# Optimization experiments

Measured on AMD Instinct MI355X. Metric: run time of the kernel, lower is better.

Reference implementation:

```python
import jax, jax.numpy as jnp
import numpy as np

D = 256; H = 8; L = 4; K = 4; AS = 2; HD = D // H
KK = K * K
LEVEL_SHAPES = [(128, 128), (64, 64), (32, 32), (16, 16)]


def _kernel_indices():
    # kernel_size=4 (even): linspace(-1.5, 1.5, 4); stack [j, i] then / K
    idx = jnp.linspace(-1.5, 1.5, K)
    ii, jj = jnp.meshgrid(idx, idx, indexing='ij')
    return jnp.stack([jj, ii], axis=-1).reshape(-1, 2) / K  # (KK, 2)


def _bilinear(vf, g, Hl, Wl):
    # vf: (b, H, Hl*Wl, HD) per-level value; g: (b, l1, H, KK, 2) in [0,1]
    # grid_sample semantics, align_corners=False, zero padding
    b, l1, h, kk, _ = g.shape
    x = g[..., 0] * Wl - 0.5
    y = g[..., 1] * Hl - 0.5
    x0 = jnp.floor(x)
    y0 = jnp.floor(y)
    acc = None
    for dx, dy in ((0, 0), (1, 0), (0, 1), (1, 1)):
        xi = x0 + dx
        yi = y0 + dy
        w = (1.0 - jnp.abs(x - xi)) * (1.0 - jnp.abs(y - yi))
        valid = (xi >= 0) & (xi < Wl) & (yi >= 0) & (yi < Hl)
        idx = (jnp.clip(yi, 0, Hl - 1) * Wl + jnp.clip(xi, 0, Wl - 1)).astype(jnp.int32)
        idx = idx.transpose(0, 2, 1, 3).reshape(b, h, l1 * kk)
        gth = jnp.take_along_axis(vf, idx[..., None], axis=2)  # (b,H,l1*kk,HD)
        ww = (w * valid).transpose(0, 2, 1, 3).reshape(b, h, l1 * kk)
        c = gth * ww[..., None]
        acc = c if acc is None else acc + c
    return acc.reshape(b, h, l1, kk, HD).transpose(0, 2, 1, 3, 4)  # (b,l1,H,kk,HD)


def setup_inputs() -> dict:
    key = jax.random.key(0)
    ks = jax.random.split(key, 9)
    b, l1 = 4, 1024
    l2 = sum(h * w for h, w in LEVEL_SHAPES)  # 21760
    query = jax.random.normal(ks[0], (b, l1, D), jnp.float32)
    value = jax.random.normal(ks[1], (b, l2, D), jnp.float32)
    centers = jax.random.uniform(ks[2], (b, l1, 2), jnp.float32)
    sizes = jax.random.uniform(ks[3], (b, l1, 2), jnp.float32) * 0.2 + 0.05
    ref_windows = jnp.concatenate([centers, sizes], axis=-1)  # (b,l1,4) cx,cy,w,h
    s = 1.0 / np.sqrt(D)
    Wv = jax.random.normal(ks[4], (D, D), jnp.float32) * s
    bv = jnp.zeros((D,), jnp.float32)
    Wo = jax.random.normal(ks[5], (D, D), jnp.float32) * s
    bo = jnp.zeros((D,), jnp.float32)
    Wbox = jax.random.normal(ks[6], (L * H * 4, D), jnp.float32) * 0.01
    bbox = jax.random.uniform(ks[7], (H * L * 4,), jnp.float32)
    Wattn = jax.random.normal(ks[8], (H * L * AS * AS, D), jnp.float32) * s
    battn = jnp.zeros((H * L * AS * AS,), jnp.float32)
    v_shape = np.array(LEVEL_SHAPES, np.int64)
    starts = np.cumsum([0] + [h * w for h, w in LEVEL_SHAPES[:-1]])
    v_start_index = np.array(starts, np.int64)
    v_mask = jnp.zeros((b, l2), bool)
    return dict(query=query, value=value, ref_windows=ref_windows, Wv=Wv, bv=bv,
                Wo=Wo, bo=bo, Wbox=Wbox, bbox=bbox, Wattn=Wattn, battn=battn,
                v_shape=v_shape, v_start_index=v_start_index, v_mask=v_mask)


def reference(query, value, ref_windows, Wv, bv, Wo, bo, Wbox, bbox, Wattn, battn,
              v_shape, v_start_index, v_mask):
    b, l1, _ = query.shape
    l2 = value.shape[1]
    # value projection + padding mask
    v = value @ Wv.T + bv
    v = jnp.where(v_mask[..., None], 0.0, v).reshape(b, l2, H, HD)
    # where to attend: offset boxes -> sampling grid (normalizer=None branch)
    off = (query @ Wbox.T + bbox).reshape(b, l1, H, L, 4)
    refw = ref_windows[:, :, None, None, :]            # (b,l1,1,1,4)
    refsz = jnp.concatenate([refw[..., 2:4], refw[..., 2:4]], axis=-1)
    boxes = refw + off / 8.0 * refsz                   # (b,l1,H,L,4)
    center = boxes[..., None, :2]
    size = boxes[..., None, 2:]
    grid = center + _kernel_indices() * jax.nn.relu(size)  # (b,l1,H,L,KK,2)
    # attention weights (attn_size grid upsampled to kernel_size by repeat_interleave)
    aw = (query @ Wattn.T + battn).reshape(b, l1, H, L, AS, AS)
    nr = K // AS
    aw = jnp.repeat(jnp.repeat(aw, nr, axis=-1), nr, axis=-2)  # (b,l1,H,L,K,K)
    sw = jax.nn.softmax(aw.reshape(b, l1, H, -1), axis=-1).reshape(b, l1, H, L, KK)
    lw = jax.nn.softmax(aw, axis=3).reshape(b, l1, H, L, KK)
    out = jnp.zeros((b, l1, H, HD), query.dtype)
    mout = jnp.zeros((b, l1, H, HD), query.dtype)
    for li in range(L):
        Hl, Wl = int(v_shape[li, 0]), int(v_shape[li, 1])
        st = int(v_start_index[li])
        vf = v[:, st:st + Hl * Wl].transpose(0, 2, 1, 3)  # (b,H,Hl*Wl,HD)
        samp = _bilinear(vf, grid[:, :, :, li], Hl, Wl)   # (b,l1,H,KK,HD)
        out = out + jnp.einsum('bqhkd,bqhk->bqhd', samp, sw[:, :, :, li])
        mout = mout + jnp.einsum('bqhkd,bqhk->bqhd', samp, lw[:, :, :, li])
    out = out.reshape(b, l1, D) @ Wo.T + bo
    mout = mout.reshape(b, l1, D) @ Wo.T + bo
    return out, mout, aw
```

## Files before the change

kernel.cpp:

```cpp
#include <hip/hip_runtime.h>
#include <hip/hip_bf16.h>


typedef __attribute__((ext_vector_type(8))) short short8;
typedef __attribute__((ext_vector_type(4))) float f32x4;
typedef __attribute__((ext_vector_type(4))) unsigned int uint4v;

__device__ __forceinline__ unsigned short f2bf(float f) {
    unsigned int u = __float_as_uint(f);
    unsigned int r = u + 0x7FFFu + ((u >> 16) & 1u);
    return (unsigned short)(r >> 16);
}
__device__ __forceinline__ unsigned int pkbf(float a, float b) {
    __hip_bfloat162 h = __float22bfloat162_rn(float2{a, b});
    return *reinterpret_cast<unsigned int*>(&h);
}
__device__ __forceinline__ short8 pack2(float4 x, float4 y) {
    uint4v u;
    u[0] = pkbf(x.x, x.y); u[1] = pkbf(x.z, x.w);
    u[2] = pkbf(y.x, y.y); u[3] = pkbf(y.z, y.w);
    return __builtin_bit_cast(short8, u);
}
__device__ __forceinline__ void gld_lds16(const float* g, float* l) {
    __builtin_amdgcn_global_load_lds(
        (const __attribute__((address_space(1))) unsigned int*)g,
        (__attribute__((address_space(3))) unsigned int*)l, 16, 0, 0);
}

__device__ __forceinline__ void storeC(float* C, size_t i, float v) { C[i] = v; }
__device__ __forceinline__ void storeC(unsigned short* C, size_t i, float v) { C[i] = f2bf(v); }

#define TILE_F 4096

template <typename OutT>
__device__ __forceinline__ void gemm_body2(
    const float* __restrict__ A, const float* __restrict__ W,
    const float* __restrict__ bias, OutT* __restrict__ C,
    int N, int bm, int bn, float* AsF, float* WsF)
{
    const int tid  = threadIdx.x;
    const int lane = tid & 63;
    const int wave = tid >> 6;
    const int wm = (wave & 1) * 64;
    const int wn = (wave >> 1) * 64;
    const int kg = lane >> 4;
    const int lm = lane & 15;

    f32x4 acc[4][4];
#pragma unroll
    for (int i = 0; i < 4; ++i)
#pragma unroll
        for (int j = 0; j < 4; ++j) {
            acc[i][j][0] = 0.f; acc[i][j][1] = 0.f;
            acc[i][j][2] = 0.f; acc[i][j][3] = 0.f;
        }

    const int g = (lane & 7) ^ (lane >> 3);
    const float* Ag = A + (size_t)(bm + 32 * wave + (lane >> 3)) * 256 + 4 * g;
    const float* Wg = W + (size_t)(bn + 32 * wave + (lane >> 3)) * 256 + 4 * g;
    const int ldsw = (32 * wave) * 32;

    const int p0 = (2 * kg) ^ (lm & 7);
    const int p1 = p0 ^ 1;
    const int abase = (wm + lm) * 8;
    const int bbase = (wn + lm) * 8;

#define STAGE_VQ(BUF, K0)                                                     \
    {                                                                         \
        _Pragma("unroll")                                                     \
        for (int j = 0; j < 4; ++j) {                                         \
            gld_lds16(Ag + (size_t)j * 8 * 256 + (K0),                        \
                      AsF + (BUF) * TILE_F + ldsw + j * 8 * 32);              \
            gld_lds16(Wg + (size_t)j * 8 * 256 + (K0),                        \
                      WsF + (BUF) * TILE_F + ldsw + j * 8 * 32);              \
        }                                                                     \
    }

#define COMPUTE_VQ(BUF)                                                       \
    {                                                                         \
        const float4* Af4 = (const float4*)(AsF + (BUF) * TILE_F);            \
        const float4* Wf4 = (const float4*)(WsF + (BUF) * TILE_F);            \
        short8 af[4], bfr[4];                                                 \
        _Pragma("unroll")                                                     \
        for (int i = 0; i < 4; ++i) {                                         \
            float4 c0 = Af4[abase + i * 128 + p0];                            \
            float4 c1 = Af4[abase + i * 128 + p1];                            \
            af[i] = pack2(c0, c1);                                            \
        }                                                                     \
        _Pragma("unroll")                                                     \
        for (int j = 0; j < 4; ++j) {                                         \
            float4 c0 = Wf4[bbase + j * 128 + p0];                            \
            float4 c1 = Wf4[bbase + j * 128 + p1];                            \
            bfr[j] = pack2(c0, c1);                                           \
        }                                                                     \
        _Pragma("unroll")                                                     \
        for (int i = 0; i < 4; ++i)                                           \
            _Pragma("unroll")                                                 \
            for (int j = 0; j < 4; ++j)                                       \
                acc[i][j] = __builtin_amdgcn_mfma_f32_16x16x32_bf16(          \
                    af[i], bfr[j], acc[i][j], 0, 0, 0);                       \
    }

    STAGE_VQ(0, 0)

    for (int it = 0; it < 7; ++it) {
        const int cur = it & 1;
        const int nxt = cur ^ 1;
        STAGE_VQ(nxt, 32 * (it + 1))
        asm volatile("s_waitcnt vmcnt(8)" ::: "memory");
        __builtin_amdgcn_s_barrier();
        COMPUTE_VQ(cur)
        asm volatile("s_waitcnt lgkmcnt(0)" ::: "memory");
        __builtin_amdgcn_s_barrier();
    }
    asm volatile("s_waitcnt vmcnt(0)" ::: "memory");
    __builtin_amdgcn_s_barrier();
    COMPUTE_VQ(1)

#undef STAGE_VQ
#undef COMPUTE_VQ

#pragma unroll
    for (int j = 0; j < 4; ++j) {
        int col = bn + wn + j * 16 + lm;
        float bcol = bias[col];
#pragma unroll
        for (int i = 0; i < 4; ++i) {
#pragma unroll
            for (int r = 0; r < 4; ++r) {
                int row = bm + wm + i * 16 + kg * 4 + r;
                storeC(C, (size_t)row * N + col, acc[i][j][r] + bcol);
            }
        }
    }
}

#define LDA 56

__device__ __forceinline__ void gemm_body_f32(
    const float* __restrict__ A, const float* __restrict__ W,
    const float* __restrict__ bias, float* __restrict__ C,
    int N, int bm, int bn, unsigned short* As, unsigned short* Ws)
{
    const int tid  = threadIdx.x;
    const int lane = tid & 63;
    const int wave = tid >> 6;
    const int wm = (wave & 1) * 64;
    const int wn = (wave >> 1) * 64;
    const int lr = tid >> 1;
    const int lh = (tid & 1) * 16;
    const int kg = lane >> 4;
    const int lm = lane & 15;

    f32x4 acc[4][4];
#pragma unroll
    for (int i = 0; i < 4; ++i)
#pragma unroll
        for (int j = 0; j < 4; ++j) {
            acc[i][j][0] = 0.f; acc[i][j][1] = 0.f;
            acc[i][j][2] = 0.f; acc[i][j][3] = 0.f;
        }

    const float* Ap = A + (size_t)(bm + lr) * 256 + lh;
    const float* Wp = W + (size_t)(bn + lr) * 256 + lh;
    unsigned short* Asp = &As[lr * LDA + lh];
    unsigned short* Wsp = &Ws[lr * LDA + lh];

    for (int k0 = 0; k0 < 256; k0 += 32) {
        float4 a0 = *(const float4*)(Ap + k0);
        float4 a1 = *(const float4*)(Ap + k0 + 4);
        float4 a2 = *(const float4*)(Ap + k0 + 8);
        float4 a3 = *(const float4*)(Ap + k0 + 12);
        float4 w0 = *(const float4*)(Wp + k0);
        float4 w1 = *(const float4*)(Wp + k0 + 4);
        float4 w2 = *(const float4*)(Wp + k0 + 8);
        float4 w3 = *(const float4*)(Wp + k0 + 12);
        __syncthreads();
        *(short8*)(Asp)     = pack2(a0, a1);
        *(short8*)(Asp + 8) = pack2(a2, a3);
        *(short8*)(Wsp)     = pack2(w0, w1);
        *(short8*)(Wsp + 8) = pack2(w2, w3);
        __syncthreads();
        short8 af[4], bfr[4];
#pragma unroll
        for (int i = 0; i < 4; ++i)
            af[i] = *(const short8*)&As[(wm + i * 16 + lm) * LDA + kg * 8];
#pragma unroll
        for (int j = 0; j < 4; ++j)
            bfr[j] = *(const short8*)&Ws[(wn + j * 16 + lm) * LDA + kg * 8];
#pragma unroll
        for (int i = 0; i < 4; ++i)
#pragma unroll
            for (int j = 0; j < 4; ++j)
                acc[i][j] = __builtin_amdgcn_mfma_f32_16x16x32_bf16(
                    af[i], bfr[j], acc[i][j], 0, 0, 0);
    }

#pragma unroll
    for (int j = 0; j < 4; ++j) {
        int col = bn + wn + j * 16 + lm;
        float bcol = bias[col];
#pragma unroll
        for (int i = 0; i < 4; ++i)
#pragma unroll
            for (int r = 0; r < 4; ++r) {
                int row = bm + wm + i * 16 + kg * 4 + r;
                C[(size_t)row * N + col] = acc[i][j][r] + bcol;
            }
    }
}

__device__ __forceinline__ void gemm_body_bf16A(
    const unsigned short* __restrict__ A, const float* __restrict__ W,
    const float* __restrict__ bias, float* __restrict__ C,
    int N, int bm, int bn, unsigned short* As, unsigned short* Ws)
{
    const int tid  = threadIdx.x;
    const int lane = tid & 63;
    const int wave = tid >> 6;
    const int wm = (wave & 1) * 64;
    const int wn = (wave >> 1) * 64;
    const int lr = tid >> 1;
    const int lh = (tid & 1) * 16;
    const int kg = lane >> 4;
    const int lm = lane & 15;

    f32x4 acc[4][4];
#pragma unroll
    for (int i = 0; i < 4; ++i)
#pragma unroll
        for (int j = 0; j < 4; ++j) {
            acc[i][j][0] = 0.f; acc[i][j][1] = 0.f;
            acc[i][j][2] = 0.f; acc[i][j][3] = 0.f;
        }

    const unsigned short* Ap = A + (size_t)(bm + lr) * 256 + lh;
    const float* Wp = W + (size_t)(bn + lr) * 256 + lh;
    unsigned short* Asp = &As[lr * LDA + lh];
    unsigned short* Wsp = &Ws[lr * LDA + lh];

    for (int k0 = 0; k0 < 256; k0 += 32) {
        uint4v a01 = *(const uint4v*)(Ap + k0);
        uint4v a23 = *(const uint4v*)(Ap + k0 + 8);
        float4 w0 = *(const float4*)(Wp + k0);
        float4 w1 = *(const float4*)(Wp + k0 + 4);
        float4 w2 = *(const float4*)(Wp + k0 + 8);
        float4 w3 = *(const float4*)(Wp + k0 + 12);
        __syncthreads();
        *(short8*)(Asp)     = __builtin_bit_cast(short8, a01);
        *(short8*)(Asp + 8) = __builtin_bit_cast(short8, a23);
        *(short8*)(Wsp)     = pack2(w0, w1);
        *(short8*)(Wsp + 8) = pack2(w2, w3);
        __syncthreads();
        short8 af[4], bfr[4];
#pragma unroll
        for (int i = 0; i < 4; ++i)
            af[i] = *(const short8*)&As[(wm + i * 16 + lm) * LDA + kg * 8];
#pragma unroll
        for (int j = 0; j < 4; ++j)
            bfr[j] = *(const short8*)&Ws[(wn + j * 16 + lm) * LDA + kg * 8];
#pragma unroll
        for (int i = 0; i < 4; ++i)
#pragma unroll
            for (int j = 0; j < 4; ++j)
                acc[i][j] = __builtin_amdgcn_mfma_f32_16x16x32_bf16(
                    af[i], bfr[j], acc[i][j], 0, 0, 0);
    }

#pragma unroll
    for (int j = 0; j < 4; ++j) {
        int col = bn + wn + j * 16 + lm;
        float bcol = bias[col];
#pragma unroll
        for (int i = 0; i < 4; ++i)
#pragma unroll
            for (int r = 0; r < 4; ++r) {
                int row = bm + wm + i * 16 + kg * 4 + r;
                C[(size_t)row * N + col] = acc[i][j][r] + bcol;
            }
    }
}

__global__ __launch_bounds__(256) void gemm_vq_kernel(
    const float* __restrict__ value, const float* __restrict__ Wv,
    const float* __restrict__ bv, unsigned short* __restrict__ v,
    const float* __restrict__ query,
    const float* __restrict__ Wbox, const float* __restrict__ bbox, float* __restrict__ off,
    const float* __restrict__ Wattn, const float* __restrict__ battn, float* __restrict__ awr)
{
    __shared__ __align__(16) char smem[65536];
    const int x = blockIdx.x;
    if (x < 1360) {
        gemm_body2<unsigned short>(value, Wv, bv, v, 256,
                                   (x >> 1) * 128, (x & 1) * 128,
                                   (float*)smem, (float*)(smem + 32768));
    } else {
        const int idx = x - 1360;
        const int bm = (idx & 31) * 128;
        unsigned short* As = (unsigned short*)smem;
        unsigned short* Ws = As + 128 * LDA;
        if (idx < 32) gemm_body_f32(query, Wbox, bbox, off, 128, bm, 0, As, Ws);
        else          gemm_body_f32(query, Wattn, battn, awr, 128, bm, 0, As, Ws);
    }
}

__global__ __launch_bounds__(256) void gemm_o_kernel(
    const unsigned short* __restrict__ A, const float* __restrict__ W,
    const float* __restrict__ bias, float* __restrict__ C)
{
    __shared__ __align__(16) unsigned short As[128 * LDA];
    __shared__ __align__(16) unsigned short Ws[128 * LDA];
    gemm_body_bf16A(A, W, bias, C, 256, blockIdx.x * 128, blockIdx.y * 128, As, Ws);
}

__global__ __launch_bounds__(512, 8) void sample_kernel(
    const unsigned short* __restrict__ v, const float* __restrict__ off,
    const float* __restrict__ awr, const float* __restrict__ refw,
    float* __restrict__ aw_out, unsigned short* __restrict__ accb)
{
    const int x  = blockIdx.x;
    const int bq = ((x & 3) << 10) | (x >> 2);
    const int b  = bq >> 10;
    const int t  = threadIdx.x;

    __shared__ float ref4[4];
    __shared__ float awl[128];
    __shared__ float bxs[128];
    __shared__ float swl[512];
    __shared__ float lwl[512];
    __shared__ int4  tp[32 * 66];

    if (t < 4)   ref4[t] = refw[bq * 4 + t];
    if (t < 128) awl[t] = awr[(size_t)bq * 128 + t];
    __syncthreads();

    if (t < 128) {
        float o = off[(size_t)bq * 128 + t];
        int comp = t & 3;
        float r0 = ref4[0], r1 = ref4[1], r2 = ref4[2], r3 = ref4[3];
        float bx;
        if (comp == 0)      bx = r0 + o * 0.125f * r2;
        else if (comp == 1) bx = r1 + o * 0.125f * r3;
        else if (comp == 2) bx = r2 + o * 0.125f * r2;
        else                bx = r3 + o * 0.125f * r3;
        bxs[t] = bx;

        const int h = t >> 4, r = t & 15;
        float a = awl[t];
        float m = a;
#pragma unroll
        for (int s = 1; s < 16; s <<= 1) m = fmaxf(m, __shfl_xor(m, s, 16));
        float se = expf(a - m);
#pragma unroll
        for (int s = 1; s < 16; s <<= 1) se += __shfl_xor(se, s, 16);
        const float inv_s = 1.0f / (4.0f * se);

        float* awq = aw_out + (size_t)bq * 512 + h * 64;
#pragma unroll
        for (int j = 0; j < 4; ++j) {
            int eidx = r * 4 + j;
            int l  = eidx >> 4;
            int ky = (eidx >> 2) & 3;
            int kx = eidx & 3;
            int pos = (ky >> 1) * 2 + (kx >> 1);
            float raw = awl[h * 16 + l * 4 + pos];
            swl[h * 64 + eidx] = expf(raw - m) * inv_s;
            int base = h * 16 + pos;
            float m2 = awl[base];
#pragma unroll
            for (int li = 1; li < 4; ++li) m2 = fmaxf(m2, awl[base + li * 4]);
            float s2 = 0.f;
#pragma unroll
            for (int li = 0; li < 4; ++li) s2 += expf(awl[base + li * 4] - m2);
            lwl[h * 64 + eidx] = expf(raw - m2) / s2;
            awq[eidx] = raw;
        }
    }
    __syncthreads();

    {
        const int STs_[4] = {0, 16384, 20480, 21504};
        int e = t;
        int eh = e >> 6, rem = e & 63, l = rem >> 4, kk = rem & 15;
        const float* bx = &bxs[eh * 16 + l * 4];
        float cx = bx[0], cy = bx[1];
        float bw = fmaxf(bx[2], 0.f), bh = fmaxf(bx[3], 0.f);
        float kx = -0.375f + 0.25f * (float)(kk & 3);
        float ky = -0.375f + 0.25f * (float)(kk >> 2);
        int Wl = 128 >> l;
        float xg = (cx + kx * bw) * (float)Wl - 0.5f;
        float yg = (cy + ky * bh) * (float)Wl - 0.5f;
        float x0f = floorf(xg), y0f = floorf(yg);
        int x0 = (int)x0f, y0 = (int)y0f;
        float fx = xg - x0f, fy = yg - y0f;
        float sww = swl[e], lww = lwl[e];
        int rowbase = b * 21760 + STs_[l];
        int4* dst = &tp[(eh * 4 + l) * 66 + kk * 4];
#pragma unroll
        for (int tap = 0; tap < 4; ++tap) {
            int dx = tap & 1, dy = tap >> 1;
            int xi = x0 + dx, yi = y0 + dy;
            float w = (dx ? fx : 1.f - fx) * (dy ? fy : 1.f - fy);
            if (xi < 0 || xi >= Wl || yi < 0 || yi >= Wl) w = 0.f;
            int xc = min(max(xi, 0), Wl - 1);
            int yc = min(max(yi, 0), Wl - 1);
            dst[tap] = int4{(rowbase + yc * Wl + xc) << 6,
                            __float_as_int(w * sww),
                            __float_as_int(w * lww), 0};
        }
    }
    __syncthreads();

    const int h    = t >> 6;
    const int lane = t & 63;
    const int l    = (lane >> 4) & 3;
    const int sub  = (lane >> 3) & 1;
    const int cl   = lane & 7;
    const uint2* vp = (const uint2*)v;
    const int choff = h * 8 + cl;
    const int4* sp = &tp[(h * 4 + l) * 66 + sub];

    float a0 = 0.f, a1 = 0.f, a2 = 0.f, a3 = 0.f;
    float m0 = 0.f, m1 = 0.f, m2 = 0.f, m3 = 0.f;
#pragma unroll 4
    for (int i = 0; i < 32; ++i) {
        int4 d = sp[2 * i];
        uint2 pv = vp[(size_t)(d.x + choff)];
        float v0 = __uint_as_float(pv.x << 16);
        float v1 = __uint_as_float(pv.x & 0xffff0000u);
        float v2 = __uint_as_float(pv.y << 16);
        float v3 = __uint_as_float(pv.y & 0xffff0000u);
        float wo = __int_as_float(d.y), wm = __int_as_float(d.z);
        a0 = fmaf(v0, wo, a0); a1 = fmaf(v1, wo, a1);
        a2 = fmaf(v2, wo, a2); a3 = fmaf(v3, wo, a3);
        m0 = fmaf(v0, wm, m0); m1 = fmaf(v1, wm, m1);
        m2 = fmaf(v2, wm, m2); m3 = fmaf(v3, wm, m3);
    }
#pragma unroll
    for (int s = 8; s <= 32; s <<= 1) {
        a0 += __shfl_xor(a0, s); a1 += __shfl_xor(a1, s);
        a2 += __shfl_xor(a2, s); a3 += __shfl_xor(a3, s);
        m0 += __shfl_xor(m0, s); m1 += __shfl_xor(m1, s);
        m2 += __shfl_xor(m2, s); m3 += __shfl_xor(m3, s);
    }
    if (lane < 8) {
        size_t base = (size_t)bq * 256 + h * 32 + cl * 4;
        *(uint2*)&accb[base] = uint2{pkbf(a0, a1), pkbf(a2, a3)};
        *(uint2*)&accb[base + (size_t)4096 * 256] = uint2{pkbf(m0, m1), pkbf(m2, m3)};
    }
}

extern "C" void kernel_launch(void* const* d_in, const int* in_sizes, int n_in,
                              void* d_out, int out_size, void* d_ws, size_t ws_size,
                              hipStream_t stream) {
    const float* query = (const float*)d_in[0];
    const float* value = (const float*)d_in[1];
    const float* refw  = (const float*)d_in[2];
    const float* Wv    = (const float*)d_in[3];
    const float* bv    = (const float*)d_in[4];
    const float* Wo    = (const float*)d_in[5];
    const float* bo    = (const float*)d_in[6];
    const float* Wbox  = (const float*)d_in[7];
    const float* bbox  = (const float*)d_in[8];
    const float* Wattn = (const float*)d_in[9];
    const float* battn = (const float*)d_in[10];

    float* out = (float*)d_out;
    float* aw_out = out + 2 * 1048576;

    unsigned short* v = (unsigned short*)d_ws;
    float* off = (float*)((char*)d_ws + 44564480);
    float* awr = off + 524288;
    unsigned short* accb = (unsigned short*)(awr + 524288);

    gemm_vq_kernel<<<1424, 256, 0, stream>>>(value, Wv, bv, v,
                                             query, Wbox, bbox, off,
                                             Wattn, battn, awr);
    sample_kernel<<<4096, 512, 0, stream>>>(v, off, awr, refw, aw_out, accb);
    gemm_o_kernel<<<dim3(64, 2), 256, 0, stream>>>(accb, Wo, bo, out);
}
```

Before: 249.5 us.

## Widen sampling gathers to 16-byte loads and restructure V-GEMM pipeline syncs

The sample kernel now has each lane gather 8 bf16 channels with a 16-byte load instead of 4 channels with an 8-byte load. Four lanes cover a head's 32 channels and four taps are processed in parallel per level, with one extra shuffle-reduction stage. This halves the gather instruction count and loop trip count but doubles accumulator registers, so the occupancy hint drops from 8 to 6. Separately, the value-projection GEMM loop is restructured to wait on all outstanding loads before each barrier, with a peeled last iteration merged into an unrolled loop.

```diff
diff --git a/kernel.cpp b/kernel.cpp
--- a/kernel.cpp
+++ b/kernel.cpp
@@ -102,21 +102,21 @@
     }
 
     STAGE_VQ(0, 0)
-
-    for (int it = 0; it < 7; ++it) {
+    asm volatile("s_waitcnt vmcnt(0)" ::: "memory");
+    __builtin_amdgcn_s_barrier();
+
+#pragma unroll 2
+    for (int it = 0; it < 8; ++it) {
         const int cur = it & 1;
         const int nxt = cur ^ 1;
-        STAGE_VQ(nxt, 32 * (it + 1))
-        asm volatile("s_waitcnt vmcnt(8)" ::: "memory");
-        __builtin_amdgcn_s_barrier();
+        if (it < 7) STAGE_VQ(nxt, 32 * (it + 1))
         COMPUTE_VQ(cur)
-        asm volatile("s_waitcnt lgkmcnt(0)" ::: "memory");
-        __builtin_amdgcn_s_barrier();
-    }
-    asm volatile("s_waitcnt vmcnt(0)" ::: "memory");
-    __builtin_amdgcn_s_barrier();
-    COMPUTE_VQ(1)
-
+        if (it < 7) {
+            asm volatile("s_waitcnt vmcnt(0) lgkmcnt(0)" ::: "memory");
+            __builtin_amdgcn_s_barrier();
+            asm volatile("" ::: "memory");
+        }
+    }
 #undef STAGE_VQ
 #undef COMPUTE_VQ
 
@@ -313,7 +313,7 @@
     gemm_body_bf16A(A, W, bias, C, 256, blockIdx.x * 128, blockIdx.y * 128, As, Ws);
 }
 
-__global__ __launch_bounds__(512, 8) void sample_kernel(
+__global__ __launch_bounds__(512, 6) void sample_kernel(
     const unsigned short* __restrict__ v, const float* __restrict__ off,
     const float* __restrict__ awr, const float* __restrict__ refw,
     float* __restrict__ aw_out, unsigned short* __restrict__ accb)
@@ -404,7 +404,7 @@
             if (xi < 0 || xi >= Wl || yi < 0 || yi >= Wl) w = 0.f;
             int xc = min(max(xi, 0), Wl - 1);
             int yc = min(max(yi, 0), Wl - 1);
-            dst[tap] = int4{(rowbase + yc * Wl + xc) << 6,
+            dst[tap] = int4{(rowbase + yc * Wl + xc) << 5,
                             __float_as_int(w * sww),
                             __float_as_int(w * lww), 0};
         }
@@ -414,39 +414,58 @@
     const int h    = t >> 6;
     const int lane = t & 63;
     const int l    = (lane >> 4) & 3;
-    const int sub  = (lane >> 3) & 1;
-    const int cl   = lane & 7;
-    const uint2* vp = (const uint2*)v;
-    const int choff = h * 8 + cl;
+    const int sub  = (lane >> 2) & 3;
+    const int cl   = lane & 3;
+    const uint4v* vp = (const uint4v*)v;
+    const int choff = h * 4 + cl;
     const int4* sp = &tp[(h * 4 + l) * 66 + sub];
 
     float a0 = 0.f, a1 = 0.f, a2 = 0.f, a3 = 0.f;
+    float a4 = 0.f, a5 = 0.f, a6 = 0.f, a7 = 0.f;
     float m0 = 0.f, m1 = 0.f, m2 = 0.f, m3 = 0.f;
+    float m4 = 0.f, m5 = 0.f, m6 = 0.f, m7 = 0.f;
 #pragma unroll 4
-    for (int i = 0; i < 32; ++i) {
-        int4 d = sp[2 * i];
-        uint2 pv = vp[(size_t)(d.x + choff)];
-        float v0 = __uint_as_float(pv.x << 16);
-        float v1 = __uint_as_float(pv.x & 0xffff0000u);
-        float v2 = __uint_as_float(pv.y << 16);
-        float v3 = __uint_as_float(pv.y & 0xffff0000u);
+    for (int i = 0; i < 16; ++i) {
+        int4 d = sp[4 * i];
+        uint4v pv = vp[(size_t)(d.x + choff)];
         float wo = __int_as_float(d.y), wm = __int_as_float(d.z);
+        float v0 = __uint_as_float(pv[0] << 16);
+        float v1 = __uint_as_float(pv[0] & 0xffff0000u);
+        float v2 = __uint_as_float(pv[1] << 16);
+        float v3 = __uint_as_float(pv[1] & 0xffff0000u);
+        float v4 = __uint_as_float(pv[2] << 16);
+        float v5 = __uint_as_float(pv[2] & 0xffff0000u);
+        float v6 = __uint_as_float(pv[3] << 16);
+        float v7 = __uint_as_float(pv[3] & 0xffff0000u);
         a0 = fmaf(v0, wo, a0); a1 = fmaf(v1, wo, a1);
         a2 = fmaf(v2, wo, a2); a3 = fmaf(v3, wo, a3);
+        a4 = fmaf(v4, wo, a4); a5 = fmaf(v5, wo, a5);
+        a6 = fmaf(v6, wo, a6); a7 = fmaf(v7, wo, a7);
         m0 = fmaf(v0, wm, m0); m1 = fmaf(v1, wm, m1);
         m2 = fmaf(v2, wm, m2); m3 = fmaf(v3, wm, m3);
-    }
-#pragma unroll
-    for (int s = 8; s <= 32; s <<= 1) {
+        m4 = fmaf(v4, wm, m4); m5 = fmaf(v5, wm, m5);
+        m6 = fmaf(v6, wm, m6); m7 = fmaf(v7, wm, m7);
+    }
+#pragma unroll
+    for (int s = 4; s <= 32; s <<= 1) {
         a0 += __shfl_xor(a0, s); a1 += __shfl_xor(a1, s);
         a2 += __shfl_xor(a2, s); a3 += __shfl_xor(a3, s);
+        a4 += __shfl_xor(a4, s); a5 += __shfl_xor(a5, s);
+        a6 += __shfl_xor(a6, s); a7 += __shfl_xor(a7, s);
         m0 += __shfl_xor(m0, s); m1 += __shfl_xor(m1, s);
         m2 += __shfl_xor(m2, s); m3 += __shfl_xor(m3, s);
-    }
-    if (lane < 8) {
-        size_t base = (size_t)bq * 256 + h * 32 + cl * 4;
-        *(uint2*)&accb[base] = uint2{pkbf(a0, a1), pkbf(a2, a3)};
-        *(uint2*)&accb[base + (size_t)4096 * 256] = uint2{pkbf(m0, m1), pkbf(m2, m3)};
+        m4 += __shfl_xor(m4, s); m5 += __shfl_xor(m5, s);
+        m6 += __shfl_xor(m6, s); m7 += __shfl_xor(m7, s);
+    }
+    if (lane < 4) {
+        size_t base = (size_t)bq * 256 + h * 32 + cl * 8;
+        uint4v ua, um;
+        ua[0] = pkbf(a0, a1); ua[1] = pkbf(a2, a3);
+        ua[2] = pkbf(a4, a5); ua[3] = pkbf(a6, a7);
+        um[0] = pkbf(m0, m1); um[1] = pkbf(m2, m3);
+        um[2] = pkbf(m4, m5); um[3] = pkbf(m6, m7);
+        *(uint4v*)&accb[base] = ua;
+        *(uint4v*)&accb[base + (size_t)4096 * 256] = um;
     }
 }
 
```

Result: slower. 255.5 us (+2.4%).

## Store projected value in head-major planes and simplify GEMM pipeline waits

Applied to the files above, without the earlier changes.

The value projection now writes its bf16 output in a per-batch, per-head planar layout (b, H, l2, 32) instead of row-major (b, l2, 256), and the sampling kernel's gather indices are updated to match. Each bilinear tap for a head then reads from a compact 64-byte row within that head's plane, which should improve locality and cache-line reuse for the gathers. The GEMM main loop is also restructured: it does a full wait after the first stage, then overlaps the next stage's load with compute and uses a single full vmcnt/lgkmcnt wait plus barrier per iteration. That single full wait may reduce how much the global loads overlap with compute compared with the old partial vmcnt(8) wait.

```diff
diff --git a/kernel.cpp b/kernel.cpp
--- a/kernel.cpp
+++ b/kernel.cpp
@@ -27,16 +27,12 @@
         (__attribute__((address_space(3))) unsigned int*)l, 16, 0, 0);
 }
 
-__device__ __forceinline__ void storeC(float* C, size_t i, float v) { C[i] = v; }
-__device__ __forceinline__ void storeC(unsigned short* C, size_t i, float v) { C[i] = f2bf(v); }
-
 #define TILE_F 4096
 
-template <typename OutT>
-__device__ __forceinline__ void gemm_body2(
+__device__ __forceinline__ void gemm_body_v(
     const float* __restrict__ A, const float* __restrict__ W,
-    const float* __restrict__ bias, OutT* __restrict__ C,
-    int N, int bm, int bn, float* AsF, float* WsF)
+    const float* __restrict__ bias, unsigned short* __restrict__ C,
+    int bm, int bn, int vb, int pbase, float* AsF, float* WsF)
 {
     const int tid  = threadIdx.x;
     const int lane = tid & 63;
@@ -102,21 +98,21 @@
     }
 
     STAGE_VQ(0, 0)
-
-    for (int it = 0; it < 7; ++it) {
+    asm volatile("s_waitcnt vmcnt(0)" ::: "memory");
+    __builtin_amdgcn_s_barrier();
+
+#pragma unroll 2
+    for (int it = 0; it < 8; ++it) {
         const int cur = it & 1;
         const int nxt = cur ^ 1;
-        STAGE_VQ(nxt, 32 * (it + 1))
-        asm volatile("s_waitcnt vmcnt(8)" ::: "memory");
-        __builtin_amdgcn_s_barrier();
+        if (it < 7) STAGE_VQ(nxt, 32 * (it + 1))
         COMPUTE_VQ(cur)
-        asm volatile("s_waitcnt lgkmcnt(0)" ::: "memory");
-        __builtin_amdgcn_s_barrier();
-    }
-    asm volatile("s_waitcnt vmcnt(0)" ::: "memory");
-    __builtin_amdgcn_s_barrier();
-    COMPUTE_VQ(1)
-
+        if (it < 7) {
+            asm volatile("s_waitcnt vmcnt(0) lgkmcnt(0)" ::: "memory");
+            __builtin_amdgcn_s_barrier();
+            asm volatile("" ::: "memory");
+        }
+    }
 #undef STAGE_VQ
 #undef COMPUTE_VQ
 
@@ -124,12 +120,15 @@
     for (int j = 0; j < 4; ++j) {
         int col = bn + wn + j * 16 + lm;
         float bcol = bias[col];
+        size_t plane = (size_t)(vb * 8 + (col >> 5)) * 21760;
+        int ch = col & 31;
 #pragma unroll
         for (int i = 0; i < 4; ++i) {
 #pragma unroll
             for (int r = 0; r < 4; ++r) {
-                int row = bm + wm + i * 16 + kg * 4 + r;
-                storeC(C, (size_t)row * N + col, acc[i][j][r] + bcol);
+                int row_local = wm + i * 16 + kg * 4 + r;
+                size_t idx = ((plane + pbase + row_local) << 5) + ch;
+                C[idx] = f2bf(acc[i][j][r] + bcol);
             }
         }
     }
@@ -291,9 +290,11 @@
     __shared__ __align__(16) char smem[65536];
     const int x = blockIdx.x;
     if (x < 1360) {
-        gemm_body2<unsigned short>(value, Wv, bv, v, 256,
-                                   (x >> 1) * 128, (x & 1) * 128,
-                                   (float*)smem, (float*)(smem + 32768));
+        const int rb = x >> 1;
+        const int vb = rb / 170;
+        const int pbase = (rb - vb * 170) * 128;
+        gemm_body_v(value, Wv, bv, v, rb * 128, (x & 1) * 128,
+                    vb, pbase, (float*)smem, (float*)(smem + 32768));
     } else {
         const int idx = x - 1360;
         const int bm = (idx & 31) * 128;
@@ -394,7 +395,7 @@
         int x0 = (int)x0f, y0 = (int)y0f;
         float fx = xg - x0f, fy = yg - y0f;
         float sww = swl[e], lww = lwl[e];
-        int rowbase = b * 21760 + STs_[l];
+        int rowbase = (b * 8 + eh) * 21760 + STs_[l];
         int4* dst = &tp[(eh * 4 + l) * 66 + kk * 4];
 #pragma unroll
         for (int tap = 0; tap < 4; ++tap) {
@@ -404,7 +405,7 @@
             if (xi < 0 || xi >= Wl || yi < 0 || yi >= Wl) w = 0.f;
             int xc = min(max(xi, 0), Wl - 1);
             int yc = min(max(yi, 0), Wl - 1);
-            dst[tap] = int4{(rowbase + yc * Wl + xc) << 6,
+            dst[tap] = int4{(rowbase + yc * Wl + xc) << 3,
                             __float_as_int(w * sww),
                             __float_as_int(w * lww), 0};
         }
@@ -417,7 +418,6 @@
     const int sub  = (lane >> 3) & 1;
     const int cl   = lane & 7;
     const uint2* vp = (const uint2*)v;
-    const int choff = h * 8 + cl;
     const int4* sp = &tp[(h * 4 + l) * 66 + sub];
 
     float a0 = 0.f, a1 = 0.f, a2 = 0.f, a3 = 0.f;
@@ -425,7 +425,7 @@
 #pragma unroll 4
     for (int i = 0; i < 32; ++i) {
         int4 d = sp[2 * i];
-        uint2 pv = vp[(size_t)(d.x + choff)];
+        uint2 pv = vp[(size_t)(d.x + cl)];
         float v0 = __uint_as_float(pv.x << 16);
         float v1 = __uint_as_float(pv.x & 0xffff0000u);
         float v2 = __uint_as_float(pv.y << 16);
```

Result: faster. 244.3 us (-2.1%).
